# Kernel tuning notes

Hardware: AMD Instinct MI355X
Metric: run time of the kernel (lower is better)

The kernel has to match this reference:

```python
import jax, jax.numpy as jnp
import numpy as np

B, N, D = 8, 1024, 256
H = 8
DH = D // H
R = 4          # relation types 0..3; adj value 4 = no relation
FF = 1024
EPS = 1e-5


def _lin(k, fan_in, shape):
    return jax.random.normal(k, shape, jnp.float32) * (1.0 / np.sqrt(fan_in))


def setup_inputs() -> dict:
    key = jax.random.key(0)
    ks = jax.random.split(key, 16)
    src = jax.random.normal(ks[0], (B, N, D), jnp.float32)
    adj_matrix = jax.random.randint(ks[1], (B, N, N), 0, 5, dtype=jnp.int32)
    Wq = _lin(ks[2], D, (D, D)); bq = jnp.zeros((D,), jnp.float32)
    Wk = _lin(ks[3], D, (D, D)); bk = jnp.zeros((D,), jnp.float32)
    Wv = _lin(ks[4], D, (R, D, D)); bv = jnp.zeros((R, D), jnp.float32)
    Wo = _lin(ks[5], D, (D, D)); bo = jnp.zeros((D,), jnp.float32)
    W1 = _lin(ks[6], D, (D, FF)); b1 = jnp.zeros((FF,), jnp.float32)
    W2 = _lin(ks[7], FF, (FF, D)); b2 = jnp.zeros((D,), jnp.float32)
    g1 = jnp.ones((D,), jnp.float32); beta1 = jnp.zeros((D,), jnp.float32)
    g2 = jnp.ones((D,), jnp.float32); beta2 = jnp.zeros((D,), jnp.float32)
    return dict(src=src, adj_matrix=adj_matrix, Wq=Wq, bq=bq, Wk=Wk, bk=bk,
                Wv=Wv, bv=bv, Wo=Wo, bo=bo, W1=W1, b1=b1, W2=W2, b2=b2,
                g1=g1, beta1=beta1, g2=g2, beta2=beta2)


def _ln(x, g, b):
    m = x.mean(-1, keepdims=True)
    v = ((x - m) ** 2).mean(-1, keepdims=True)
    return (x - m) * jax.lax.rsqrt(v + EPS) * g + b


def reference(src, adj_matrix, Wq, bq, Wk, bk, Wv, bv, Wo, bo, W1, b1, W2, b2, g1, beta1, g2, beta2):
    Bb, Nn, Dm = src.shape
    h, dh = H, Dm // H
    q = (src @ Wq + bq).reshape(Bb, Nn, h, dh).transpose(0, 2, 1, 3)  # (B,H,N,dh)
    k = (src @ Wk + bk).reshape(Bb, Nn, h, dh).transpose(0, 2, 1, 3)
    scores = jnp.einsum('bhid,bhjd->bhij', q, k) / np.sqrt(dh)
    attn = jax.nn.softmax(scores, axis=-1)                             # (B,H,N,N)
    out = jnp.zeros_like(q)
    for r in range(Wv.shape[0]):  # small fixed relation loop, matches module
        v_r = (src @ Wv[r] + bv[r]).reshape(Bb, Nn, h, dh).transpose(0, 2, 1, 3)
        mask = (adj_matrix == r)[:, None]                              # (B,1,N,N)
        out = out + jnp.einsum('bhij,bhjd->bhid', attn * mask, v_r)
    attn_out = out.transpose(0, 2, 1, 3).reshape(Bb, Nn, Dm) @ Wo + bo
    x = _ln(src + attn_out, g1, beta1)
    ff = jax.nn.gelu(x @ W1 + b1, approximate=False) @ W2 + b2
    return _ln(x + ff, g2, beta2)
```

## Files before the change

### kernel.cpp

```cpp
#include <hip/hip_runtime.h>
#include <hip/hip_bf16.h>
#include <cmath>

constexpr int CB  = 8;
constexpr int CN  = 1024;
constexpr int CD  = 256;
constexpr int CH  = 8;
constexpr int CDH = 32;
constexpr int CR  = 4;
constexpr int CFF = 1024;
constexpr float CEPS = 1e-5f;
constexpr size_t SZH = (size_t)CB * CH * CN * CDH;

#define MODE_QK    0
#define MODE_FFN1  2
#define MODE_VT    4

typedef float v4f __attribute__((ext_vector_type(4)));
typedef short v8s __attribute__((ext_vector_type(8)));

static __device__ __forceinline__ short f2bf(float f) {
    unsigned u = __builtin_bit_cast(unsigned, f);
    u += 0x7fff + ((u >> 16) & 1);
    return (short)(u >> 16);
}

static __device__ __forceinline__ void async_copy16(const void* g, void* l) {
    __builtin_amdgcn_global_load_lds(
        (const __attribute__((address_space(1))) void*)g,
        (__attribute__((address_space(3))) void*)l, 16, 0, 0);
}

template<int BM, int BN, int MODE>
__device__ __forceinline__ void gemm_body(
    const short* __restrict__ A, const short* __restrict__ Bw,
    const float* __restrict__ biasv, void* __restrict__ dest,
    int M, int K, int Nw, int bx, int by, short* smem)
{
    constexpr int WTM = BM / 2, WTN = BN / 2;
    constexpr int TM = WTM / 16, TN = WTN / 16;
    short* As = smem;
    short* Bs = smem + 2 * BM * 32;

    const int t    = threadIdx.x;
    const int lane = t & 63;
    const int w    = t >> 6;
    const int quad = lane >> 4, l15 = lane & 15;
    const int wm = w >> 1, wn = w & 1;
    const int m0 = bx * BM, n0 = by * BN;

    const int srow = lane >> 2;
    const int scol = (lane & 3) * 8;

    v4f acc[TM][TN];
    #pragma unroll
    for (int i = 0; i < TM; ++i)
        #pragma unroll
        for (int j = 0; j < TN; ++j) acc[i][j] = (v4f){0.f, 0.f, 0.f, 0.f};

    const int NK = K >> 5;

    auto stage = [&](int buf, int kt) {
        #pragma unroll
        for (int u = 0; u < BM / 64; ++u) {
            const int e0 = (w * (BM / 64) + u) * 512;
            const int row = (e0 >> 5) + srow;
            async_copy16(A + (size_t)(m0 + row) * K + kt + scol,
                         &As[buf * BM * 32 + e0]);
        }
        #pragma unroll
        for (int u = 0; u < BN / 64; ++u) {
            const int e0 = (w * (BN / 64) + u) * 512;
            const int row = (e0 >> 5) + srow;
            async_copy16(Bw + (size_t)(n0 + row) * K + kt + scol,
                         &Bs[buf * BN * 32 + e0]);
        }
    };

    stage(0, 0);

    for (int it = 0; it < NK; ++it) {
        __syncthreads();
        if (it + 1 < NK) stage((it + 1) & 1, (it + 1) << 5);

        const int buf = it & 1;
        v8s af[TM], bfr[TN];
        #pragma unroll
        for (int i = 0; i < TM; ++i)
            af[i] = *(const v8s*)&As[buf * BM * 32 +
                                     (wm * WTM + i * 16 + l15) * 32 + quad * 8];
        #pragma unroll
        for (int j = 0; j < TN; ++j)
            bfr[j] = *(const v8s*)&Bs[buf * BN * 32 +
                                      (wn * WTN + j * 16 + l15) * 32 + quad * 8];
        #pragma unroll
        for (int i = 0; i < TM; ++i)
            #pragma unroll
            for (int j = 0; j < TN; ++j)
                acc[i][j] = __builtin_amdgcn_mfma_f32_16x16x32_bf16(
                    af[i], bfr[j], acc[i][j], 0, 0, 0);
    }

    #pragma unroll
    for (int i = 0; i < TM; ++i) {
        #pragma unroll
        for (int j = 0; j < TN; ++j) {
            const int mb = m0 + wm * WTM + i * 16 + quad * 4;
            const int n  = n0 + wn * WTN + j * 16 + l15;
            float vals[4];
            if (MODE == MODE_VT) {
                #pragma unroll
                for (int rr = 0; rr < 4; ++rr) vals[rr] = acc[i][j][rr] + biasv[mb + rr];
            } else {
                #pragma unroll
                for (int rr = 0; rr < 4; ++rr) vals[rr] = acc[i][j][rr] + biasv[n];
            }

            if (MODE == MODE_QK) {
                const int b = mb >> 10, ii0 = mb & 1023;
                const int plane = n >> 8, nn = n & 255;
                const int h = nn >> 5, d = nn & 31;
                #pragma unroll
                for (int rr = 0; rr < 4; ++rr)
                    ((short*)dest)[(size_t)plane * SZH +
                        (((size_t)(b * CH + h)) * CN + ii0 + rr) * CDH + d] =
                        f2bf(vals[rr]);
            } else if (MODE == MODE_VT) {
                const int b = n >> 10, ii = n & 1023;
                #pragma unroll
                for (int rr = 0; rr < 4; ++rr) {
                    const int m = mb + rr;
                    const int r2 = m >> 8, hd = m & 255;
                    const int h = hd >> 5, d = hd & 31;
                    ((short*)dest)[2 * SZH +
                        (((size_t)(r2 * 64 + b * CH + h)) * CDH + d) * CN + ii] =
                        f2bf(vals[rr]);
                }
            } else {
                #pragma unroll
                for (int rr = 0; rr < 4; ++rr) {
                    const size_t idx = (size_t)(mb + rr) * Nw + n;
                    const float xx = vals[rr];
                    const float E = exp2f(2.302217f * (xx + 0.044715f * xx * xx * xx));
                    ((short*)dest)[idx] = f2bf(xx * E / (E + 1.f));
                }
            }
        }
    }
}

template<int BM, int BN, int MODE>
__global__ __launch_bounds__(256)
void gemm_mfma(const short* __restrict__ A, const short* __restrict__ Bw,
               const float* __restrict__ biasv, void* __restrict__ dest,
               int M, int K, int Nw)
{
    extern __shared__ short smem[];
    gemm_body<BM, BN, MODE>(A, Bw, biasv, dest, M, K, Nw,
                            blockIdx.x, blockIdx.y, smem);
}

__global__ __launch_bounds__(256)
void proj_kernel(const short* __restrict__ src_bf, const short* __restrict__ wqkvT,
                 const float* __restrict__ bpack, short* __restrict__ qkv,
                 const int* __restrict__ adj, unsigned char* __restrict__ adj8)
{
    extern __shared__ short smem[];
    const int g = blockIdx.x;
    if (g < 512) {
        gemm_body<64, 128, MODE_QK>(src_bf, wqkvT, bpack, qkv,
                                    8192, 256, 512, g >> 2, g & 3, smem);
    } else if (g < 1536) {
        const int h2 = g - 512;
        gemm_body<64, 128, MODE_VT>(wqkvT + 512 * 256, src_bf, bpack + 512,
                                    qkv, 1024, 256, 8192, h2 & 15, h2 >> 4, smem);
    } else {
        const int n4 = CB * CN * CN / 4;
        for (int i = (g - 1536) * 256 + threadIdx.x; i < n4; i += 512 * 256) {
            const int4 vv = ((const int4*)adj)[i];
            uchar4 c;
            c.x = (unsigned char)vv.x; c.y = (unsigned char)vv.y;
            c.z = (unsigned char)vv.z; c.w = (unsigned char)vv.w;
            ((uchar4*)adj8)[i] = c;
        }
    }
}

template<bool WRITE_BF>
__global__ __launch_bounds__(256)
void gemm_ln32(const short* __restrict__ A, const short* __restrict__ Bw,
               const float* __restrict__ biasv, const float* __restrict__ add,
               const float* __restrict__ gw, const float* __restrict__ be,
               float* __restrict__ outf, short* __restrict__ outb, int K)
{
    __shared__ short As[2][32 * 32];
    __shared__ short Bs[2][256 * 32];
    __shared__ float redS[2][16][2], redQ[2][16][2];

    const int t    = threadIdx.x;
    const int lane = t & 63;
    const int w    = t >> 6;
    const int quad = lane >> 4, l15 = lane & 15;
    const int wr   = w >> 1;
    const int wg   = w & 1;
    const int m0   = blockIdx.x * 32;

    const int srow = lane >> 2;
    const int scol = (lane & 3) * 8;

    v4f acc[8];
    #pragma unroll
    for (int j = 0; j < 8; ++j) acc[j] = (v4f){0.f, 0.f, 0.f, 0.f};

    const int NK = K >> 5;

    auto stage = [&](int buf, int kt) {
        if (w < 2)
            async_copy16(A + (size_t)(m0 + 16 * w + srow) * K + kt + scol,
                         &As[buf][w * 512]);
        #pragma unroll
        for (int u = 0; u < 4; ++u) {
            const int e0 = (w * 4 + u) * 512;
            async_copy16(Bw + (size_t)((e0 >> 5) + srow) * K + kt + scol,
                         &Bs[buf][e0]);
        }
    };

    stage(0, 0);

    for (int it = 0; it < NK; ++it) {
        __syncthreads();
        if (it + 1 < NK) stage((it + 1) & 1, (it + 1) << 5);

        const int buf = it & 1;
        const v8s af = *(const v8s*)&As[buf][(16 * wr + l15) * 32 + quad * 8];
        #pragma unroll
        for (int j = 0; j < 8; ++j) {
            const v8s bfr = *(const v8s*)&Bs[buf][(wg * 128 + 16 * j + l15) * 32 + quad * 8];
            acc[j] = __builtin_amdgcn_mfma_f32_16x16x32_bf16(af, bfr, acc[j], 0, 0, 0);
        }
    }

    float v[4][8];
    #pragma unroll
    for (int rr = 0; rr < 4; ++rr) {
        const int row = m0 + 16 * wr + quad * 4 + rr;
        float s = 0.f, sq = 0.f;
        #pragma unroll
        for (int j = 0; j < 8; ++j) {
            const int n = wg * 128 + 16 * j + l15;
            const float x = acc[j][rr] + biasv[n] + add[(size_t)row * CD + n];
            v[rr][j] = x;
            s += x; sq += x * x;
        }
        #pragma unroll
        for (int off = 1; off < 16; off <<= 1) {
            s  += __shfl_xor(s, off);
            sq += __shfl_xor(sq, off);
        }
        if (l15 == 0) {
            redS[wr][quad * 4 + rr][wg] = s;
            redQ[wr][quad * 4 + rr][wg] = sq;
        }
    }
    __syncthreads();

    #pragma unroll
    for (int rr = 0; rr < 4; ++rr) {
        const int r16 = quad * 4 + rr;
        const int row = m0 + 16 * wr + r16;
        const float s  = redS[wr][r16][0] + redS[wr][r16][1];
        const float sq = redQ[wr][r16][0] + redQ[wr][r16][1];
        const float mean = s * (1.f / CD);
        const float var  = sq * (1.f / CD) - mean * mean;
        const float rstd = rsqrtf(var + CEPS);
        #pragma unroll
        for (int j = 0; j < 8; ++j) {
            const int n = wg * 128 + 16 * j + l15;
            const float y = (v[rr][j] - mean) * rstd * gw[n] + be[n];
            outf[(size_t)row * CD + n] = y;
            if (WRITE_BF) outb[(size_t)row * CD + n] = f2bf(y);
        }
    }
}

__global__ __launch_bounds__(256)
void prep(const float* __restrict__ src,
          const float* __restrict__ Wq, const float* __restrict__ Wk,
          const float* __restrict__ Wv, const float* __restrict__ Wo,
          const float* __restrict__ W1, const float* __restrict__ W2,
          const float* __restrict__ bq, const float* __restrict__ bk,
          const float* __restrict__ bv, const float* __restrict__ bo,
          const float* __restrict__ b1, const float* __restrict__ b2,
          short* __restrict__ src_bf,
          short* __restrict__ wqkvT, short* __restrict__ woT,
          short* __restrict__ w1T, short* __restrict__ w2T,
          float* __restrict__ bpack)
{
    __shared__ float tile[64][65];
    const int bx = blockIdx.x, t = threadIdx.x;
    if (bx < 2048) {
        const int i = bx * 256 + t;
        const float4 v = ((const float4*)src)[i];
        short4 o;
        o.x = f2bf(v.x); o.y = f2bf(v.y); o.z = f2bf(v.z); o.w = f2bf(v.w);
        ((short4*)src_bf)[i] = o;
    } else if (bx < 2288) {
        const int tt = bx - 2048;
        const float* S; short* D;
        int Sstride, Dstride, k0, srccol, dstrow;
        if (tt < 96) {
            const int tk = tt & 3, tn = tt >> 2;
            const int ng = tn * 64;
            Sstride = 256; Dstride = 256; k0 = tk * 64;
            dstrow = tn * 64; D = wqkvT;
            if (ng < 256)      { S = Wq; srccol = ng; }
            else if (ng < 512) { S = Wk; srccol = ng - 256; }
            else { const int r = (ng - 512) >> 8;
                   S = Wv + (size_t)r * 65536; srccol = (ng - 512) & 255; }
        } else if (tt < 112) {
            const int u = tt - 96, tk = u & 3, tn = u >> 2;
            S = Wo; Sstride = 256; D = woT; Dstride = 256;
            k0 = tk * 64; srccol = tn * 64; dstrow = tn * 64;
        } else if (tt < 176) {
            const int u = tt - 112, tk = u & 3, tn = u >> 2;
            S = W1; Sstride = 1024; D = w1T; Dstride = 256;
            k0 = tk * 64; srccol = tn * 64; dstrow = tn * 64;
        } else {
            const int u = tt - 176, tk = u & 15, tn = u >> 4;
            S = W2; Sstride = 256; D = w2T; Dstride = 1024;
            k0 = tk * 64; srccol = tn * 64; dstrow = tn * 64;
        }
        #pragma unroll
        for (int u2 = 0; u2 < 4; ++u2) {
            const int kl = (t >> 4) + u2 * 16;
            const int nl = (t & 15) * 4;
            const float4 v = *(const float4*)&S[(size_t)(k0 + kl) * Sstride + srccol + nl];
            tile[kl][nl + 0] = v.x; tile[kl][nl + 1] = v.y;
            tile[kl][nl + 2] = v.z; tile[kl][nl + 3] = v.w;
        }
        __syncthreads();
        #pragma unroll
        for (int u2 = 0; u2 < 4; ++u2) {
            const int nl = (t >> 4) + u2 * 16;
            const int kl = (t & 15) * 4;
            short4 o;
            o.x = f2bf(tile[kl + 0][nl]); o.y = f2bf(tile[kl + 1][nl]);
            o.z = f2bf(tile[kl + 2][nl]); o.w = f2bf(tile[kl + 3][nl]);
            *(short4*)&D[(size_t)(dstrow + nl) * Dstride + k0 + kl] = o;
        }
    } else {
        const int idx = (bx - 2288) * 256 + t;
        float bvv;
        if (idx < 256)       bvv = bq[idx];
        else if (idx < 512)  bvv = bk[idx - 256];
        else if (idx < 1536) bvv = bv[idx - 512];
        else if (idx < 1792) bvv = bo[idx - 1536];
        else if (idx < 2816) bvv = b1[idx - 1792];
        else                 bvv = b2[idx - 2816];
        bpack[idx] = bvv;
    }
}

__global__ __launch_bounds__(256)
void attn_mfma(const short* __restrict__ qg, const short* __restrict__ kg,
               const short* __restrict__ vt, const unsigned char* __restrict__ adj8,
               short* __restrict__ outh)
{
    __shared__ __align__(16) short ks[64 * 32];
    __shared__ __align__(16) short vtile[4][32][72];
    __shared__ __align__(16) short ps[64][68];
    __shared__ __align__(16) unsigned char adjs[64][72];
    __shared__ int lut[64][4];

    const int t    = threadIdx.x;
    const int lane = t & 63;
    const int w    = t >> 6;
    const int quad = lane >> 4;
    const int l15  = lane & 15;
    const int i0   = blockIdx.x * 64;
    const int h    = blockIdx.y;
    const int b    = blockIdx.z;
    const int bhh  = b * CH + h;
    const size_t bh = (size_t)bhh;

    if (t < 64) {
        const int b0 = t & 7, b1 = t >> 3;
        #pragma unroll
        for (int r = 0; r < 4; ++r) {
            const int lo = (b0 == r) ? 0x0100 : 0x0c0c;
            const int hi = (b1 == r) ? 0x0302 : 0x0c0c;
            lut[t][r] = lo | (hi << 16);
        }
    }

    const v8s qfrag = *(const v8s*)&qg[(bh * CN + i0 + 16 * w + l15) * CDH + quad * 8];

    v4f oacc[2];
    oacc[0] = (v4f){0.f, 0.f, 0.f, 0.f};
    oacc[1] = (v4f){0.f, 0.f, 0.f, 0.f};
    float plsum[4] = {0.f, 0.f, 0.f, 0.f};

    const float cs = 0.25503480f;
    const int arow = 16 * w + l15;

    const int srow = lane >> 2;
    const int scol = (lane & 3) * 8;
    const int vd0  = lane >> 3;
    const int vc   = (lane & 7) * 8;
    const short* vplane = vt + (((size_t)(w * 64 + bhh)) * CDH) * CN;
    const int aro = t >> 2;
    const int aco = (t & 3) * 16;

    for (int jt = 0; jt < 16; ++jt) {
        const int j0 = jt * 64;
        __syncthreads();

        async_copy16(kg + (bh * CN + j0 + 16 * w + srow) * CDH + scol,
                     &ks[(16 * w + srow) * 32]);
        #pragma unroll
        for (int it = 0; it < 4; ++it) {
            const int d = vd0 + 8 * it;
            const v8s vv = *(const v8s*)&vplane[(size_t)d * CN + j0 + vc];
            *(v8s*)&vtile[w][d][vc] = vv;
        }
        const int4 av = *(const int4*)&adj8[((size_t)b * CN + i0 + aro) * CN + j0 + aco];
        *(int4*)&adjs[aro][aco] = av;
        __syncthreads();

        v4f sacc[4];
        #pragma unroll
        for (int jb = 0; jb < 4; ++jb) {
            const v8s kfrag = *(const v8s*)&ks[(16 * jb + l15) * 32 + quad * 8];
            sacc[jb] = __builtin_amdgcn_mfma_f32_16x16x32_bf16(
                qfrag, kfrag, (v4f){0.f, 0.f, 0.f, 0.f}, 0, 0, 0);
        }

        #pragma unroll
        for (int rr = 0; rr < 4; ++rr) {
            const int prow = 16 * w + quad * 4 + rr;
            float p[4];
            #pragma unroll
            for (int jb = 0; jb < 4; ++jb) p[jb] = exp2f(cs * sacc[jb][rr]);
            plsum[rr] += (p[0] + p[1]) + (p[2] + p[3]);
            #pragma unroll
            for (int jb = 0; jb < 4; ++jb)
                ps[prow][16 * jb + l15] = f2bf(p[jb]);
        }

        #pragma unroll
        for (int kb = 0; kb < 2; ++kb) {
            const int2 p0 = *(const int2*)&ps[arow][32 * kb + quad * 8];
            const int2 p1 = *(const int2*)&ps[arow][32 * kb + quad * 8 + 4];
            const int2 ab = *(const int2*)&adjs[arow][32 * kb + quad * 8];
            int pf[4][4];
            #pragma unroll
            for (int half = 0; half < 2; ++half) {
                const unsigned a = (unsigned)(half ? ab.y : ab.x);
                const int P0 = half ? p1.x : p0.x;
                const int P1 = half ? p1.y : p0.y;
                const int idxA = (a & 7) | ((a >> 5) & 0x38);
                const int idxB = ((a >> 16) & 7) | ((a >> 21) & 0x38);
                const int4 selA = *(const int4*)&lut[idxA][0];
                const int4 selB = *(const int4*)&lut[idxB][0];
                pf[0][half * 2 + 0] = __builtin_amdgcn_perm(P0, P0, selA.x);
                pf[1][half * 2 + 0] = __builtin_amdgcn_perm(P0, P0, selA.y);
                pf[2][half * 2 + 0] = __builtin_amdgcn_perm(P0, P0, selA.z);
                pf[3][half * 2 + 0] = __builtin_amdgcn_perm(P0, P0, selA.w);
                pf[0][half * 2 + 1] = __builtin_amdgcn_perm(P1, P1, selB.x);
                pf[1][half * 2 + 1] = __builtin_amdgcn_perm(P1, P1, selB.y);
                pf[2][half * 2 + 1] = __builtin_amdgcn_perm(P1, P1, selB.z);
                pf[3][half * 2 + 1] = __builtin_amdgcn_perm(P1, P1, selB.w);
            }
            #pragma unroll
            for (int r = 0; r < 4; ++r) {
                const v8s pfr = __builtin_bit_cast(v8s,
                    make_int4(pf[r][0], pf[r][1], pf[r][2], pf[r][3]));
                #pragma unroll
                for (int cb = 0; cb < 2; ++cb) {
                    const v8s vfrag = *(const v8s*)&vtile[r][16 * cb + l15][32 * kb + quad * 8];
                    oacc[cb] = __builtin_amdgcn_mfma_f32_16x16x32_bf16(
                        pfr, vfrag, oacc[cb], 0, 0, 0);
                }
            }
        }
    }

    #pragma unroll
    for (int rr = 0; rr < 4; ++rr) {
        float l = plsum[rr];
        #pragma unroll
        for (int off = 1; off < 16; off <<= 1) l += __shfl_xor(l, off);
        const float inv = 1.f / l;
        const int row = i0 + 16 * w + quad * 4 + rr;
        #pragma unroll
        for (int cb = 0; cb < 2; ++cb)
            outh[((size_t)b * CN + row) * CD + h * CDH + 16 * cb + l15] =
                f2bf(oacc[cb][rr] * inv);
    }
}

extern "C" void kernel_launch(void* const* d_in, const int* in_sizes, int n_in,
                              void* d_out, int out_size, void* d_ws, size_t ws_size,
                              hipStream_t stream)
{
    const float* src = (const float*)d_in[0];
    const int*   adj = (const int*)d_in[1];
    const float* Wq  = (const float*)d_in[2];
    const float* bq  = (const float*)d_in[3];
    const float* Wk  = (const float*)d_in[4];
    const float* bk  = (const float*)d_in[5];
    const float* Wv  = (const float*)d_in[6];
    const float* bv  = (const float*)d_in[7];
    const float* Wo  = (const float*)d_in[8];
    const float* bo  = (const float*)d_in[9];
    const float* W1  = (const float*)d_in[10];
    const float* b1  = (const float*)d_in[11];
    const float* W2  = (const float*)d_in[12];
    const float* b2  = (const float*)d_in[13];
    const float* g1  = (const float*)d_in[14];
    const float* be1 = (const float*)d_in[15];
    const float* g2  = (const float*)d_in[16];
    const float* be2 = (const float*)d_in[17];
    float* out = (float*)d_out;

    char* wsb = (char*)d_ws;
    const size_t MB = (size_t)1 << 20;

    unsigned char* adj8 = (unsigned char*)(wsb);
    short* qkv_bf = (short*)(wsb + 8 * MB);
    short* src_bf = (short*)(wsb + 32 * MB);
    short* wqkvT  = (short*)(wsb + 36 * MB);
    short* woT    = (short*)(wsb + 36 * MB + 768 * 1024);
    short* w1T    = (short*)(wsb + 36 * MB + 896 * 1024);
    short* w2T    = (short*)(wsb + 36 * MB + 1408 * 1024);
    float* bpack  = (float*)(wsb + 36 * MB + 1920 * 1024);
    short* heads_bf = (short*)(wsb + 38 * MB);
    float* xres   = (float*)(wsb + 42 * MB);
    short* x_bf   = (short*)(wsb + 32 * MB);
    short* h1_bf  = (short*)(wsb + 16 * MB);

    const int M = CB * CN;
    dim3 blk(256);

    prep<<<dim3(2300), blk, 0, stream>>>(src, Wq, Wk, Wv, Wo, W1, W2,
        bq, bk, bv, bo, b1, b2, src_bf, wqkvT, woT, w1T, w2T, bpack);

    proj_kernel<<<dim3(2048), blk, 24576, stream>>>(
        src_bf, wqkvT, bpack, qkv_bf, adj, adj8);

    attn_mfma<<<dim3(CN / 64, CH, CB), blk, 0, stream>>>(
        qkv_bf, qkv_bf + SZH, qkv_bf + 2 * SZH, adj8, heads_bf);

    gemm_ln32<true><<<dim3(M / 32), blk, 0, stream>>>(
        heads_bf, woT, bpack + 1536, src, g1, be1, xres, x_bf, CD);

    gemm_mfma<64, 128, MODE_FFN1><<<dim3(M / 64, CFF / 128), blk, 24576, stream>>>(
        x_bf, w1T, bpack + 1792, h1_bf, M, CD, CFF);

    gemm_ln32<false><<<dim3(M / 32), blk, 0, stream>>>(
        h1_bf, w2T, bpack + 2816, xres, g2, be2, out, nullptr, CFF);
}
```

Baseline: 246.1 us.

## Pack adjacency to 4 bits and prefetch next K/V/adj tile in attention

The adjacency conversion now packs two relation codes per byte (4-bit nibbles), which halves the adjacency bytes written by the projection kernel and read by attention. The attention loop double-buffers the K tile and loads the next iteration's V and adjacency values into registers before computing the current tile. This hides global load latency behind the MFMA and softmax work. The cost is extra registers for the prefetch, which may lower occupancy, and the LUT index is now built from nibbles.

Result: faster. 238.1 us (-3.2%).

```diff
diff --git a/kernel.cpp b/kernel.cpp
--- a/kernel.cpp
+++ b/kernel.cpp
@@ -163,7 +163,7 @@
 __global__ __launch_bounds__(256)
 void proj_kernel(const short* __restrict__ src_bf, const short* __restrict__ wqkvT,
                  const float* __restrict__ bpack, short* __restrict__ qkv,
-                 const int* __restrict__ adj, unsigned char* __restrict__ adj8)
+                 const int* __restrict__ adj, unsigned char* __restrict__ adj4)
 {
     extern __shared__ short smem[];
     const int g = blockIdx.x;
@@ -175,13 +175,16 @@
         gemm_body<64, 128, MODE_VT>(wqkvT + 512 * 256, src_bf, bpack + 512,
                                     qkv, 1024, 256, 8192, h2 & 15, h2 >> 4, smem);
     } else {
-        const int n4 = CB * CN * CN / 4;
-        for (int i = (g - 1536) * 256 + threadIdx.x; i < n4; i += 512 * 256) {
-            const int4 vv = ((const int4*)adj)[i];
-            uchar4 c;
-            c.x = (unsigned char)vv.x; c.y = (unsigned char)vv.y;
-            c.z = (unsigned char)vv.z; c.w = (unsigned char)vv.w;
-            ((uchar4*)adj8)[i] = c;
+        const int nout = CB * CN * CN / 8;
+        for (int i = (g - 1536) * 256 + threadIdx.x; i < nout; i += 512 * 256) {
+            const int4 a0 = ((const int4*)adj)[2 * i];
+            const int4 a1 = ((const int4*)adj)[2 * i + 1];
+            const unsigned p =
+                (unsigned)(a0.x & 0xf)        | ((unsigned)(a0.y & 0xf) << 4)  |
+                ((unsigned)(a0.z & 0xf) << 8) | ((unsigned)(a0.w & 0xf) << 12) |
+                ((unsigned)(a1.x & 0xf) << 16)| ((unsigned)(a1.y & 0xf) << 20) |
+                ((unsigned)(a1.z & 0xf) << 24)| ((unsigned)(a1.w & 0xf) << 28);
+            ((unsigned*)adj4)[i] = p;
         }
     }
 }
@@ -364,13 +367,13 @@
 
 __global__ __launch_bounds__(256)
 void attn_mfma(const short* __restrict__ qg, const short* __restrict__ kg,
-               const short* __restrict__ vt, const unsigned char* __restrict__ adj8,
+               const short* __restrict__ vt, const unsigned char* __restrict__ adj4,
                short* __restrict__ outh)
 {
-    __shared__ __align__(16) short ks[64 * 32];
+    __shared__ __align__(16) short ks[2][64 * 32];
     __shared__ __align__(16) short vtile[4][32][72];
     __shared__ __align__(16) short ps[64][68];
-    __shared__ __align__(16) unsigned char adjs[64][72];
+    __shared__ __align__(16) unsigned char adjs[64][40];
     __shared__ int lut[64][4];
 
     const int t    = threadIdx.x;
@@ -409,29 +412,43 @@
     const int vd0  = lane >> 3;
     const int vc   = (lane & 7) * 8;
     const short* vplane = vt + (((size_t)(w * 64 + bhh)) * CDH) * CN;
-    const int aro = t >> 2;
-    const int aco = (t & 3) * 16;
+    const unsigned char* adjg =
+        adj4 + ((size_t)(b * CN) + i0 + (t >> 2)) * (CN / 2) + (t & 3) * 8;
+
+    v8s vpre[4];
+    int2 apre;
+
+    async_copy16(kg + (bh * CN + 16 * w + srow) * CDH + scol,
+                 &ks[0][(16 * w + srow) * 32]);
+    #pragma unroll
+    for (int it = 0; it < 4; ++it)
+        vpre[it] = *(const v8s*)&vplane[(size_t)(vd0 + 8 * it) * CN + vc];
+    apre = *(const int2*)adjg;
 
     for (int jt = 0; jt < 16; ++jt) {
-        const int j0 = jt * 64;
         __syncthreads();
 
-        async_copy16(kg + (bh * CN + j0 + 16 * w + srow) * CDH + scol,
-                     &ks[(16 * w + srow) * 32]);
-        #pragma unroll
-        for (int it = 0; it < 4; ++it) {
-            const int d = vd0 + 8 * it;
-            const v8s vv = *(const v8s*)&vplane[(size_t)d * CN + j0 + vc];
-            *(v8s*)&vtile[w][d][vc] = vv;
-        }
-        const int4 av = *(const int4*)&adj8[((size_t)b * CN + i0 + aro) * CN + j0 + aco];
-        *(int4*)&adjs[aro][aco] = av;
+        #pragma unroll
+        for (int it = 0; it < 4; ++it)
+            *(v8s*)&vtile[w][vd0 + 8 * it][vc] = vpre[it];
+        *(int2*)&adjs[t >> 2][(t & 3) * 8] = apre;
         __syncthreads();
 
+        if (jt + 1 < 16) {
+            const int j1 = (jt + 1) * 64;
+            async_copy16(kg + (bh * CN + j1 + 16 * w + srow) * CDH + scol,
+                         &ks[(jt + 1) & 1][(16 * w + srow) * 32]);
+            #pragma unroll
+            for (int it = 0; it < 4; ++it)
+                vpre[it] = *(const v8s*)&vplane[(size_t)(vd0 + 8 * it) * CN + j1 + vc];
+            apre = *(const int2*)(adjg + (jt + 1) * 32);
+        }
+
+        const short* ksb = ks[jt & 1];
         v4f sacc[4];
         #pragma unroll
         for (int jb = 0; jb < 4; ++jb) {
-            const v8s kfrag = *(const v8s*)&ks[(16 * jb + l15) * 32 + quad * 8];
+            const v8s kfrag = *(const v8s*)&ksb[(16 * jb + l15) * 32 + quad * 8];
             sacc[jb] = __builtin_amdgcn_mfma_f32_16x16x32_bf16(
                 qfrag, kfrag, (v4f){0.f, 0.f, 0.f, 0.f}, 0, 0, 0);
         }
@@ -450,27 +467,19 @@
 
         #pragma unroll
         for (int kb = 0; kb < 2; ++kb) {
-            const int2 p0 = *(const int2*)&ps[arow][32 * kb + quad * 8];
-            const int2 p1 = *(const int2*)&ps[arow][32 * kb + quad * 8 + 4];
-            const int2 ab = *(const int2*)&adjs[arow][32 * kb + quad * 8];
+            const int4 praw = *(const int4*)&ps[arow][32 * kb + quad * 8];
+            const int ab32 = *(const int*)&adjs[arow][16 * kb + quad * 4];
+            const int P[4] = {praw.x, praw.y, praw.z, praw.w};
             int pf[4][4];
             #pragma unroll
-            for (int half = 0; half < 2; ++half) {
-                const unsigned a = (unsigned)(half ? ab.y : ab.x);
-                const int P0 = half ? p1.x : p0.x;
-                const int P1 = half ? p1.y : p0.y;
-                const int idxA = (a & 7) | ((a >> 5) & 0x38);
-                const int idxB = ((a >> 16) & 7) | ((a >> 21) & 0x38);
-                const int4 selA = *(const int4*)&lut[idxA][0];
-                const int4 selB = *(const int4*)&lut[idxB][0];
-                pf[0][half * 2 + 0] = __builtin_amdgcn_perm(P0, P0, selA.x);
-                pf[1][half * 2 + 0] = __builtin_amdgcn_perm(P0, P0, selA.y);
-                pf[2][half * 2 + 0] = __builtin_amdgcn_perm(P0, P0, selA.z);
-                pf[3][half * 2 + 0] = __builtin_amdgcn_perm(P0, P0, selA.w);
-                pf[0][half * 2 + 1] = __builtin_amdgcn_perm(P1, P1, selB.x);
-                pf[1][half * 2 + 1] = __builtin_amdgcn_perm(P1, P1, selB.y);
-                pf[2][half * 2 + 1] = __builtin_amdgcn_perm(P1, P1, selB.z);
-                pf[3][half * 2 + 1] = __builtin_amdgcn_perm(P1, P1, selB.w);
+            for (int u = 0; u < 4; ++u) {
+                const int byte = (ab32 >> (8 * u)) & 0xff;
+                const int idx = (byte & 7) | ((byte >> 1) & 0x38);
+                const int4 sel = *(const int4*)&lut[idx][0];
+                pf[0][u] = __builtin_amdgcn_perm(P[u], P[u], sel.x);
+                pf[1][u] = __builtin_amdgcn_perm(P[u], P[u], sel.y);
+                pf[2][u] = __builtin_amdgcn_perm(P[u], P[u], sel.z);
+                pf[3][u] = __builtin_amdgcn_perm(P[u], P[u], sel.w);
             }
             #pragma unroll
             for (int r = 0; r < 4; ++r) {
@@ -527,7 +536,7 @@
     char* wsb = (char*)d_ws;
     const size_t MB = (size_t)1 << 20;
 
-    unsigned char* adj8 = (unsigned char*)(wsb);
+    unsigned char* adj4 = (unsigned char*)(wsb);
     short* qkv_bf = (short*)(wsb + 8 * MB);
     short* src_bf = (short*)(wsb + 32 * MB);
     short* wqkvT  = (short*)(wsb + 36 * MB);
@@ -547,10 +556,10 @@
         bq, bk, bv, bo, b1, b2, src_bf, wqkvT, woT, w1T, w2T, bpack);
 
     proj_kernel<<<dim3(2048), blk, 24576, stream>>>(
-        src_bf, wqkvT, bpack, qkv_bf, adj, adj8);
+        src_bf, wqkvT, bpack, qkv_bf, adj, adj4);
 
     attn_mfma<<<dim3(CN / 64, CH, CB), blk, 0, stream>>>(
-        qkv_bf, qkv_bf + SZH, qkv_bf + 2 * SZH, adj8, heads_bf);
+        qkv_bf, qkv_bf + SZH, qkv_bf + 2 * SZH, adj4, heads_bf);
 
     gemm_ln32<true><<<dim3(M / 32), blk, 0, stream>>>(
         heads_bf, woT, bpack + 1536, src, g1, be1, xres, x_bf, CD);
```
